# Performance work log

Measured on AMD Instinct MI355X. Metric: run time of the kernel, lower is better.

## Reference

```python
import jax, jax.numpy as jnp
import numpy as np


def apply_rope(x):
    # x: [b, h, n, d], d even
    b, h, n, d = x.shape
    half = d // 2
    freqs = jnp.arange(0, half, dtype=x.dtype) / half
    theta = 1.0 / 10000 ** freqs                       # [half]
    positions = jnp.arange(n, dtype=x.dtype)
    angles = positions[:, None] * theta[None, :]       # [n, half]
    cos = jnp.cos(angles)[None, None, :, :]
    sin = jnp.sin(angles)[None, None, :, :]
    x1 = x[..., ::2]
    x2 = x[..., 1::2]
    r1 = x1 * cos - x2 * sin
    r2 = x1 * sin + x2 * cos
    # interleave r1, r2 back into even/odd lanes
    return jnp.stack([r1, r2], axis=-1).reshape(b, h, n, d)


def setup_inputs() -> dict:
    key = jax.random.key(0)
    ks = jax.random.split(key, 4)
    B, N, D = 2, 2048, 1024
    x = jax.random.normal(ks[0], (B, N, D), dtype=jnp.float32)
    w_qkv = jax.random.normal(ks[1], (D, 3 * D), dtype=jnp.float32) * (1.0 / np.sqrt(D))
    b_qkv = jnp.zeros((3 * D,), dtype=jnp.float32)
    w_out = jax.random.normal(ks[2], (D, D), dtype=jnp.float32) * (1.0 / np.sqrt(D))
    b_out = jnp.zeros((D,), dtype=jnp.float32)
    return {"x": x, "w_qkv": w_qkv, "b_qkv": b_qkv, "w_out": w_out, "b_out": b_out}


def reference(x, w_qkv, b_qkv, w_out, b_out):
    B, N, D = x.shape
    H = 16
    hd = D // H
    qkv = x @ w_qkv + b_qkv                            # [B, N, 3D]
    q, k, v = jnp.split(qkv, 3, axis=-1)
    # [B, N, D] -> [B, H, N, hd]
    to_heads = lambda t: t.reshape(B, N, H, hd).transpose(0, 2, 1, 3)
    q, k, v = to_heads(q), to_heads(k), to_heads(v)
    # ELU+1 feature map (applied BEFORE RoPE, as in source)
    q = jax.nn.elu(q) + 1
    k = jax.nn.elu(k) + 1
    rot_q = apply_rope(q)
    rot_k = apply_rope(k)
    attn_num = jnp.einsum('bhid,bhjd->bhij', rot_q, rot_k)   # [B,H,N,N]
    attn_denom = jnp.einsum('bhid,bhjd->bhij', q, k)         # [B,H,N,N]
    attn_weights = attn_num / attn_denom
    # dropout deterministic (train=False)
    out = jnp.einsum('bhij,bhjd->bhid', attn_weights, v)     # [B,H,N,hd]
    out = out.transpose(0, 2, 1, 3).reshape(B, N, D)
    return out @ w_out + b_out
```

## Files before the change

kernel.cpp:

```cpp
#include <hip/hip_runtime.h>
#include <hip/hip_bf16.h>

#define B_   2
#define N_   2048
#define D_   1024
#define H_   16
#define HD   64
#define HALF 32
#define M_   (B_*N_)
#define DQKV (3*D_)

typedef __bf16 bf16x8 __attribute__((ext_vector_type(8)));
typedef float  f32x4  __attribute__((ext_vector_type(4)));
typedef float  f32x16 __attribute__((ext_vector_type(16)));

__device__ __forceinline__ bf16x8 ldfrag(const char* tile, int row, int ch) {
    return *(const bf16x8*)(tile + row * 128 + (((ch) ^ (row & 7)) << 4));
}
__device__ __forceinline__ void stfrag16(char* tile, int row, int ch, uint4 v) {
    *(uint4*)(tile + row * 128 + (((ch) ^ (row & 7)) << 4)) = v;
}

__device__ __forceinline__ unsigned pack2(float a, float b) {
    union { __hip_bfloat16 h; unsigned short s; } x, y;
    x.h = __float2bfloat16(a); y.h = __float2bfloat16(b);
    return (unsigned)x.s | ((unsigned)y.s << 16);
}

__global__ __launch_bounds__(256) void k_tables(float* __restrict__ cos_t,
                                                float* __restrict__ sin_t) {
    int i = blockIdx.x * 256 + threadIdx.x;
    if (i >= N_ * HALF) return;
    int n = i / HALF, j = i % HALF;
    float theta = powf(10000.f, -(float)j / (float)HALF);
    float ang = (float)n * theta;
    cos_t[i] = cosf(ang);
    sin_t[i] = sinf(ang);
}

__global__ __launch_bounds__(256) void k_cvt_x(const float* __restrict__ x,
                                               __hip_bfloat16* __restrict__ xb) {
    int i = blockIdx.x * 256 + threadIdx.x;
    float4 v = ((const float4*)x)[i];
    union { ushort4 u; __hip_bfloat16 h[4]; } o;
    o.h[0] = __float2bfloat16(v.x); o.h[1] = __float2bfloat16(v.y);
    o.h[2] = __float2bfloat16(v.z); o.h[3] = __float2bfloat16(v.w);
    ((ushort4*)xb)[i] = o.u;
}

__global__ __launch_bounds__(256) void k_cvt_t(const float* __restrict__ w,
                                               __hip_bfloat16* __restrict__ wt, int ncols) {
    __shared__ float tile[32][33];
    int n0 = blockIdx.x * 32, k0 = blockIdx.y * 32;
    int tx = threadIdx.x & 31, ty = threadIdx.x >> 5;
#pragma unroll
    for (int i = 0; i < 32; i += 8)
        tile[ty + i][tx] = w[(size_t)(k0 + ty + i) * ncols + n0 + tx];
    __syncthreads();
#pragma unroll
    for (int i = 0; i < 32; i += 8)
        wt[(size_t)(n0 + ty + i) * 1024 + k0 + tx] = __float2bfloat16(tile[tx][ty + i]);
}

__global__ __launch_bounds__(256) void k_qkv(
        const __hip_bfloat16* __restrict__ xb, const __hip_bfloat16* __restrict__ wqT,
        const float* __restrict__ bias,
        const float* __restrict__ cos_t, const float* __restrict__ sin_t,
        __hip_bfloat16* __restrict__ qf, __hip_bfloat16* __restrict__ kf,
        __hip_bfloat16* __restrict__ rq, __hip_bfloat16* __restrict__ rk,
        __hip_bfloat16* __restrict__ vt) {
    __shared__ __align__(16) char sA[128 * 128];
    __shared__ __align__(16) char sB[128 * 128];

    const int t    = threadIdx.x;
    const int m0   = blockIdx.y * 128;
    const int n0w  = blockIdx.x * 128;
    const int lane = t & 63;
    const int lrow = lane & 15;
    const int lgrp = lane >> 4;
    const int wid  = t >> 6;
    const int wr   = wid >> 1;
    const int wc   = wid & 1;

    f32x4 acc[4][4] = {};

    for (int kt = 0; kt < D_ / 64; ++kt) {
        const int k0 = kt * 64;
        __syncthreads();
#pragma unroll
        for (int it = 0; it < 4; ++it) {
            int slot = it * 256 + t;
            int r = slot >> 3, c = slot & 7;
            uint4 av = *(const uint4*)(xb  + (size_t)(m0  + r) * D_ + k0 + c * 8);
            uint4 bv = *(const uint4*)(wqT + (size_t)(n0w + r) * D_ + k0 + c * 8);
            stfrag16(sA, r, c, av);
            stfrag16(sB, r, c, bv);
        }
        __syncthreads();

        bf16x8 bfr[4][2];
#pragma unroll
        for (int fn = 0; fn < 4; ++fn) {
            bfr[fn][0] = ldfrag(sB, wc * 64 + fn * 16 + lrow, lgrp);
            bfr[fn][1] = ldfrag(sB, wc * 64 + fn * 16 + lrow, 4 + lgrp);
        }
#pragma unroll
        for (int fm = 0; fm < 4; ++fm) {
            bf16x8 a0 = ldfrag(sA, wr * 64 + fm * 16 + lrow, lgrp);
            bf16x8 a1 = ldfrag(sA, wr * 64 + fm * 16 + lrow, 4 + lgrp);
#pragma unroll
            for (int fn = 0; fn < 4; ++fn) {
                acc[fm][fn] = __builtin_amdgcn_mfma_f32_16x16x32_bf16(a0, bfr[fn][0], acc[fm][fn], 0, 0, 0);
                acc[fm][fn] = __builtin_amdgcn_mfma_f32_16x16x32_bf16(a1, bfr[fn][1], acc[fm][fn], 0, 0, 0);
            }
        }
    }

#pragma unroll
    for (int fn = 0; fn < 4; ++fn) {
        int c   = n0w + wc * 64 + fn * 16 + lrow;
        int sec = c >> 10;
        int cc  = c & 1023;
        int h   = cc >> 6, dd = cc & 63;
        float bia = bias[c];
#pragma unroll
        for (int fm = 0; fm < 4; ++fm) {
            int mb = m0 + wr * 64 + fm * 16 + lgrp * 4;
            int b  = mb >> 11;
            int n  = mb & (N_ - 1);
            if (sec == 2) {
                union { ushort4 u; __hip_bfloat16 hh[4]; } pk;
#pragma unroll
                for (int r = 0; r < 4; ++r)
                    pk.hh[r] = __float2bfloat16(acc[fm][fn][r] + bia);
                *(ushort4*)(vt + ((size_t)(b * H_ + h) * HD + dd) * N_ + n) = pk.u;
            } else {
#pragma unroll
                for (int r = 0; r < 4; ++r) {
                    float val = acc[fm][fn][r] + bia;
                    float e  = val > 0.f ? val + 1.f : __expf(val);
                    float ep = __shfl_xor(e, 1);
                    int pj = dd >> 1;
                    float cs = cos_t[(n + r) * HALF + pj];
                    float sn = sin_t[(n + r) * HALF + pj];
                    float rv = (dd & 1) ? (ep * sn + e * cs) : (e * cs - ep * sn);
                    size_t o = ((size_t)(b * H_ + h) * N_ + n + r) * HD + dd;
                    if (sec == 0) { qf[o] = __float2bfloat16(e); rq[o] = __float2bfloat16(rv); }
                    else          { kf[o] = __float2bfloat16(e); rk[o] = __float2bfloat16(rv); }
                }
            }
        }
    }
}

__global__ __launch_bounds__(256, 1) void k_attn(
        const __hip_bfloat16* __restrict__ qf, const __hip_bfloat16* __restrict__ kf,
        const __hip_bfloat16* __restrict__ rq, const __hip_bfloat16* __restrict__ rk,
        const __hip_bfloat16* __restrict__ vt, __hip_bfloat16* __restrict__ ctxb) {
    __shared__ __align__(16) char sbuf[2][3 * 8192];

    const int t    = threadIdx.x;
    const int lane = t & 63;
    const int l31  = lane & 31;
    const int h    = lane >> 5;
    const int w    = t >> 6;

    const int bid = blockIdx.x;
    const int swz = (bid & 7) * 32 + (bid >> 3);
    const int bh  = swz >> 3;
    const int q0  = (swz & 7) * 256;
    const size_t base = (size_t)bh * (N_ * HD);
    const int q0w = q0 + w * 64;

    bf16x8 bq[2][4], bqe[2][4];
#pragma unroll
    for (int qb = 0; qb < 2; ++qb)
#pragma unroll
        for (int kc = 0; kc < 4; ++kc) {
            int row = q0w + qb * 32 + l31;
            int col = kc * 16 + h * 8;
            bq [qb][kc] = *(const bf16x8*)(rq + base + (size_t)row * HD + col);
            bqe[qb][kc] = *(const bf16x8*)(qf + base + (size_t)row * HD + col);
        }

    uint4 st[6];
    {
#pragma unroll
        for (int it = 0; it < 6; ++it) {
            int slot = it * 256 + t, ci = slot & 511, row = ci >> 3, cs = ci & 7;
            int cg = cs ^ (row & 7);
            const char* g;
            if (it < 2)      g = (const char*)(rk + base + (size_t)row * HD) + cg * 16;
            else if (it < 4) g = (const char*)(kf + base + (size_t)row * HD) + cg * 16;
            else             g = (const char*)(vt + base + (size_t)row * N_) + cg * 16;
            st[it] = *(const uint4*)g;
        }
#pragma unroll
        for (int it = 0; it < 6; ++it) {
            int slot = it * 256 + t, ci = slot & 511, row = ci >> 3, cs = ci & 7;
            *(uint4*)(sbuf[0] + (it >> 1) * 8192 + row * 128 + cs * 16) = st[it];
        }
    }
    __syncthreads();

    f32x16 o[2][2] = {};

    for (int kt = 0; kt < 32; ++kt) {
        const int cur = kt & 1;
        const char* Rk = sbuf[cur];
        const char* Ke = sbuf[cur] + 8192;
        const char* Vt = sbuf[cur] + 16384;

        if (kt + 1 < 32) {
            const int k0n = (kt + 1) * 64;
#pragma unroll
            for (int it = 0; it < 6; ++it) {
                int slot = it * 256 + t, ci = slot & 511, row = ci >> 3, cs = ci & 7;
                int cg = cs ^ (row & 7);
                const char* g;
                if (it < 2)      g = (const char*)(rk + base + (size_t)(k0n + row) * HD) + cg * 16;
                else if (it < 4) g = (const char*)(kf + base + (size_t)(k0n + row) * HD) + cg * 16;
                else             g = (const char*)(vt + base + (size_t)row * N_ + k0n) + cg * 16;
                st[it] = *(const uint4*)g;
            }
        }

        bf16x8 wa[2][4];
#pragma unroll
        for (int qb = 0; qb < 2; ++qb) {
#pragma unroll
            for (int kb = 0; kb < 2; ++kb) {
                f32x16 num = {}, den = {};
#pragma unroll
                for (int kc = 0; kc < 4; ++kc) {
                    bf16x8 ark = ldfrag(Rk, kb * 32 + l31, kc * 2 + h);
                    num = __builtin_amdgcn_mfma_f32_32x32x16_bf16(ark, bq[qb][kc], num, 0, 0, 0);
                }
#pragma unroll
                for (int kc = 0; kc < 4; ++kc) {
                    bf16x8 ake = ldfrag(Ke, kb * 32 + l31, kc * 2 + h);
                    den = __builtin_amdgcn_mfma_f32_32x32x16_bf16(ake, bqe[qb][kc], den, 0, 0, 0);
                }
                unsigned u0 = pack2(num[0]  * __builtin_amdgcn_rcpf(den[0]),
                                    num[1]  * __builtin_amdgcn_rcpf(den[1]));
                unsigned u1 = pack2(num[2]  * __builtin_amdgcn_rcpf(den[2]),
                                    num[3]  * __builtin_amdgcn_rcpf(den[3]));
                unsigned u2 = pack2(num[4]  * __builtin_amdgcn_rcpf(den[4]),
                                    num[5]  * __builtin_amdgcn_rcpf(den[5]));
                unsigned u3 = pack2(num[6]  * __builtin_amdgcn_rcpf(den[6]),
                                    num[7]  * __builtin_amdgcn_rcpf(den[7]));
                unsigned u4 = pack2(num[8]  * __builtin_amdgcn_rcpf(den[8]),
                                    num[9]  * __builtin_amdgcn_rcpf(den[9]));
                unsigned u5 = pack2(num[10] * __builtin_amdgcn_rcpf(den[10]),
                                    num[11] * __builtin_amdgcn_rcpf(den[11]));
                unsigned u6 = pack2(num[12] * __builtin_amdgcn_rcpf(den[12]),
                                    num[13] * __builtin_amdgcn_rcpf(den[13]));
                unsigned u7 = pack2(num[14] * __builtin_amdgcn_rcpf(den[14]),
                                    num[15] * __builtin_amdgcn_rcpf(den[15]));
                asm volatile("v_permlane32_swap_b32 %0, %1" : "+v"(u0), "+v"(u2));
                asm volatile("v_permlane32_swap_b32 %0, %1" : "+v"(u1), "+v"(u3));
                asm volatile("v_permlane32_swap_b32 %0, %1" : "+v"(u4), "+v"(u6));
                asm volatile("v_permlane32_swap_b32 %0, %1" : "+v"(u5), "+v"(u7));
                union { unsigned uu[4]; bf16x8 v; } f0, f1;
                f0.uu[0] = u0; f0.uu[1] = u1; f0.uu[2] = u2; f0.uu[3] = u3;
                f1.uu[0] = u4; f1.uu[1] = u5; f1.uu[2] = u6; f1.uu[3] = u7;
                wa[qb][kb * 2 + 0] = f0.v;
                wa[qb][kb * 2 + 1] = f1.v;
            }
        }

#pragma unroll
        for (int qb = 0; qb < 2; ++qb)
#pragma unroll
            for (int db = 0; db < 2; ++db)
#pragma unroll
                for (int kc = 0; kc < 4; ++kc) {
                    bf16x8 bv = ldfrag(Vt, db * 32 + l31, kc * 2 + h);
                    o[qb][db] = __builtin_amdgcn_mfma_f32_32x32x16_bf16(wa[qb][kc], bv, o[qb][db], 0, 0, 0);
                }

        if (kt + 1 < 32) {
#pragma unroll
            for (int it = 0; it < 6; ++it) {
                int slot = it * 256 + t, ci = slot & 511, row = ci >> 3, cs = ci & 7;
                *(uint4*)(sbuf[cur ^ 1] + (it >> 1) * 8192 + row * 128 + cs * 16) = st[it];
            }
        }
        __syncthreads();
    }

#pragma unroll
    for (int qb = 0; qb < 2; ++qb)
#pragma unroll
        for (int db = 0; db < 2; ++db)
#pragma unroll
            for (int r = 0; r < 16; ++r) {
                int qq = q0w + qb * 32 + (r & 3) + 8 * (r >> 2) + 4 * h;
                int dv = db * 32 + l31;
                ctxb[base + (size_t)qq * HD + dv] = __float2bfloat16(o[qb][db][r]);
            }
}

__global__ __launch_bounds__(256) void k_proj(
        const __hip_bfloat16* __restrict__ ctxb, const __hip_bfloat16* __restrict__ woT,
        const float* __restrict__ bias, float* __restrict__ out) {
    __shared__ __align__(16) char sA[128 * 128];
    __shared__ __align__(16) char sB[128 * 128];

    const int t    = threadIdx.x;
    const int m0   = blockIdx.y * 128;
    const int n0w  = blockIdx.x * 128;
    const int lane = t & 63;
    const int lrow = lane & 15;
    const int lgrp = lane >> 4;
    const int wid  = t >> 6;
    const int wr   = wid >> 1;
    const int wc   = wid & 1;

    f32x4 acc[4][4] = {};

    for (int kt = 0; kt < D_ / 64; ++kt) {
        const int k0 = kt * 64;
        const int hh = k0 >> 6;
        __syncthreads();
#pragma unroll
        for (int it = 0; it < 4; ++it) {
            int slot = it * 256 + t;
            int r = slot >> 3, c = slot & 7;
            int m = m0 + r;
            int b = m >> 11, n = m & (N_ - 1);
            uint4 av = *(const uint4*)(ctxb + ((size_t)(b * H_ + hh) * N_ + n) * HD + c * 8);
            uint4 bv = *(const uint4*)(woT + (size_t)(n0w + r) * D_ + k0 + c * 8);
            stfrag16(sA, r, c, av);
            stfrag16(sB, r, c, bv);
        }
        __syncthreads();

        bf16x8 bfr[4][2];
#pragma unroll
        for (int fn = 0; fn < 4; ++fn) {
            bfr[fn][0] = ldfrag(sB, wc * 64 + fn * 16 + lrow, lgrp);
            bfr[fn][1] = ldfrag(sB, wc * 64 + fn * 16 + lrow, 4 + lgrp);
        }
#pragma unroll
        for (int fm = 0; fm < 4; ++fm) {
            bf16x8 a0 = ldfrag(sA, wr * 64 + fm * 16 + lrow, lgrp);
            bf16x8 a1 = ldfrag(sA, wr * 64 + fm * 16 + lrow, 4 + lgrp);
#pragma unroll
            for (int fn = 0; fn < 4; ++fn) {
                acc[fm][fn] = __builtin_amdgcn_mfma_f32_16x16x32_bf16(a0, bfr[fn][0], acc[fm][fn], 0, 0, 0);
                acc[fm][fn] = __builtin_amdgcn_mfma_f32_16x16x32_bf16(a1, bfr[fn][1], acc[fm][fn], 0, 0, 0);
            }
        }
    }

#pragma unroll
    for (int fn = 0; fn < 4; ++fn) {
        int c = n0w + wc * 64 + fn * 16 + lrow;
        float bia = bias[c];
#pragma unroll
        for (int fm = 0; fm < 4; ++fm) {
            int m = m0 + wr * 64 + fm * 16 + lgrp * 4;
#pragma unroll
            for (int r = 0; r < 4; ++r)
                out[(size_t)(m + r) * D_ + c] = acc[fm][fn][r] + bia;
        }
    }
}

extern "C" void kernel_launch(void* const* d_in, const int* in_sizes, int n_in,
                              void* d_out, int out_size, void* d_ws, size_t ws_size,
                              hipStream_t stream) {
    const float* x     = (const float*)d_in[0];
    const float* w_qkv = (const float*)d_in[1];
    const float* b_qkv = (const float*)d_in[2];
    const float* w_out = (const float*)d_in[3];
    const float* b_out = (const float*)d_in[4];
    float* out = (float*)d_out;

    char* ws = (char*)d_ws;
    const size_t TAB  = (size_t)N_ * HALF * sizeof(float);
    const size_t HARR = (size_t)B_ * H_ * N_ * HD * 2;
    float* cos_t = (float*)ws;
    float* sin_t = (float*)(ws + TAB);
    char* p = ws + 2 * TAB;
    __hip_bfloat16* qf  = (__hip_bfloat16*)(p);            p += HARR;
    __hip_bfloat16* kf  = (__hip_bfloat16*)(p);            p += HARR;
    __hip_bfloat16* rq  = (__hip_bfloat16*)(p);            p += HARR;
    __hip_bfloat16* rk  = (__hip_bfloat16*)(p);            p += HARR;
    __hip_bfloat16* vt  = (__hip_bfloat16*)(p);            p += HARR;
    __hip_bfloat16* xb  = (__hip_bfloat16*)(p);            p += HARR;
    __hip_bfloat16* ctxb = xb;
    __hip_bfloat16* wqT = (__hip_bfloat16*)(p);            p += (size_t)DQKV * D_ * 2;
    __hip_bfloat16* woT = (__hip_bfloat16*)(p);            p += (size_t)D_ * D_ * 2;

    hipLaunchKernelGGL(k_tables, dim3((N_ * HALF + 255) / 256), dim3(256), 0, stream,
                       cos_t, sin_t);
    hipLaunchKernelGGL(k_cvt_x, dim3(M_ * D_ / 4 / 256), dim3(256), 0, stream, x, xb);
    hipLaunchKernelGGL(k_cvt_t, dim3(DQKV / 32, D_ / 32), dim3(256), 0, stream,
                       w_qkv, wqT, DQKV);
    hipLaunchKernelGGL(k_cvt_t, dim3(D_ / 32, D_ / 32), dim3(256), 0, stream,
                       w_out, woT, D_);
    hipLaunchKernelGGL(k_qkv, dim3(DQKV / 128, M_ / 128), dim3(256), 0, stream,
                       xb, wqT, b_qkv, cos_t, sin_t, qf, kf, rq, rk, vt);
    hipLaunchKernelGGL(k_attn, dim3(256), dim3(256), 0, stream,
                       qf, kf, rq, rk, vt, ctxb);
    hipLaunchKernelGGL(k_proj, dim3(D_ / 128, M_ / 128), dim3(256), 0, stream,
                       ctxb, woT, b_out, out);
}
```

Baseline: 188.5 us.

## Split attention key range across warps, load K/V fragments directly from global

The attention kernel now launches twice as many blocks, each covering 128 queries. Two warps per query tile split the key range between them (split-K), and their partial outputs are combined through shared memory at the end. The double-buffered shared-memory staging of K/V tiles and its per-iteration barriers are removed. MFMA fragments are now read straight from global memory (via cache), and launch bounds allow two blocks per CU, aiming for more parallelism and occupancy. In exchange, K/V reuse across warps now relies on L1/L2 instead of LDS, and loads are less coalesced.

```diff
diff --git a/kernel.cpp b/kernel.cpp
--- a/kernel.cpp
+++ b/kernel.cpp
@@ -153,24 +153,26 @@
     }
 }
 
-__global__ __launch_bounds__(256, 1) void k_attn(
+__global__ __launch_bounds__(256, 2) void k_attn(
         const __hip_bfloat16* __restrict__ qf, const __hip_bfloat16* __restrict__ kf,
         const __hip_bfloat16* __restrict__ rq, const __hip_bfloat16* __restrict__ rk,
         const __hip_bfloat16* __restrict__ vt, __hip_bfloat16* __restrict__ ctxb) {
-    __shared__ __align__(16) char sbuf[2][3 * 8192];
+    __shared__ float sred[2][4096];
 
     const int t    = threadIdx.x;
     const int lane = t & 63;
     const int l31  = lane & 31;
     const int h    = lane >> 5;
     const int w    = t >> 6;
+    const int qw   = w & 1;
+    const int ks   = w >> 1;
 
     const int bid = blockIdx.x;
-    const int swz = (bid & 7) * 32 + (bid >> 3);
-    const int bh  = swz >> 3;
-    const int q0  = (swz & 7) * 256;
+    const int swz = (bid & 7) * 64 + (bid >> 3);
+    const int bh  = swz >> 4;
+    const int q0  = (swz & 15) * 128;
     const size_t base = (size_t)bh * (N_ * HD);
-    const int q0w = q0 + w * 64;
+    const int q0w = q0 + qw * 64;
 
     bf16x8 bq[2][4], bqe[2][4];
 #pragma unroll
@@ -183,64 +185,31 @@
             bqe[qb][kc] = *(const bf16x8*)(qf + base + (size_t)row * HD + col);
         }
 
-    uint4 st[6];
-    {
-#pragma unroll
-        for (int it = 0; it < 6; ++it) {
-            int slot = it * 256 + t, ci = slot & 511, row = ci >> 3, cs = ci & 7;
-            int cg = cs ^ (row & 7);
-            const char* g;
-            if (it < 2)      g = (const char*)(rk + base + (size_t)row * HD) + cg * 16;
-            else if (it < 4) g = (const char*)(kf + base + (size_t)row * HD) + cg * 16;
-            else             g = (const char*)(vt + base + (size_t)row * N_) + cg * 16;
-            st[it] = *(const uint4*)g;
-        }
-#pragma unroll
-        for (int it = 0; it < 6; ++it) {
-            int slot = it * 256 + t, ci = slot & 511, row = ci >> 3, cs = ci & 7;
-            *(uint4*)(sbuf[0] + (it >> 1) * 8192 + row * 128 + cs * 16) = st[it];
-        }
-    }
-    __syncthreads();
-
     f32x16 o[2][2] = {};
 
-    for (int kt = 0; kt < 32; ++kt) {
-        const int cur = kt & 1;
-        const char* Rk = sbuf[cur];
-        const char* Ke = sbuf[cur] + 8192;
-        const char* Vt = sbuf[cur] + 16384;
-
-        if (kt + 1 < 32) {
-            const int k0n = (kt + 1) * 64;
-#pragma unroll
-            for (int it = 0; it < 6; ++it) {
-                int slot = it * 256 + t, ci = slot & 511, row = ci >> 3, cs = ci & 7;
-                int cg = cs ^ (row & 7);
-                const char* g;
-                if (it < 2)      g = (const char*)(rk + base + (size_t)(k0n + row) * HD) + cg * 16;
-                else if (it < 4) g = (const char*)(kf + base + (size_t)(k0n + row) * HD) + cg * 16;
-                else             g = (const char*)(vt + base + (size_t)row * N_ + k0n) + cg * 16;
-                st[it] = *(const uint4*)g;
-            }
-        }
+    for (int r = 0; r < 16; ++r) {
+        const int k0 = (2 * r + ks) * 64;
+        const __hip_bfloat16* pk = rk + base + (size_t)k0 * HD + h * 8;
+        const __hip_bfloat16* pe = kf + base + (size_t)k0 * HD + h * 8;
 
         bf16x8 wa[2][4];
 #pragma unroll
-        for (int qb = 0; qb < 2; ++qb) {
-#pragma unroll
-            for (int kb = 0; kb < 2; ++kb) {
+        for (int kb = 0; kb < 2; ++kb) {
+            bf16x8 ark[4], ake[4];
+#pragma unroll
+            for (int kc = 0; kc < 4; ++kc) {
+                ark[kc] = *(const bf16x8*)(pk + (size_t)(kb * 32 + l31) * HD + kc * 16);
+                ake[kc] = *(const bf16x8*)(pe + (size_t)(kb * 32 + l31) * HD + kc * 16);
+            }
+#pragma unroll
+            for (int qb = 0; qb < 2; ++qb) {
                 f32x16 num = {}, den = {};
 #pragma unroll
-                for (int kc = 0; kc < 4; ++kc) {
-                    bf16x8 ark = ldfrag(Rk, kb * 32 + l31, kc * 2 + h);
-                    num = __builtin_amdgcn_mfma_f32_32x32x16_bf16(ark, bq[qb][kc], num, 0, 0, 0);
-                }
-#pragma unroll
-                for (int kc = 0; kc < 4; ++kc) {
-                    bf16x8 ake = ldfrag(Ke, kb * 32 + l31, kc * 2 + h);
-                    den = __builtin_amdgcn_mfma_f32_32x32x16_bf16(ake, bqe[qb][kc], den, 0, 0, 0);
-                }
+                for (int kc = 0; kc < 4; ++kc)
+                    num = __builtin_amdgcn_mfma_f32_32x32x16_bf16(ark[kc], bq[qb][kc], num, 0, 0, 0);
+#pragma unroll
+                for (int kc = 0; kc < 4; ++kc)
+                    den = __builtin_amdgcn_mfma_f32_32x32x16_bf16(ake[kc], bqe[qb][kc], den, 0, 0, 0);
                 unsigned u0 = pack2(num[0]  * __builtin_amdgcn_rcpf(den[0]),
                                     num[1]  * __builtin_amdgcn_rcpf(den[1]));
                 unsigned u1 = pack2(num[2]  * __builtin_amdgcn_rcpf(den[2]),
@@ -270,35 +239,42 @@
         }
 
 #pragma unroll
+        for (int db = 0; db < 2; ++db) {
+            bf16x8 bv[4];
+#pragma unroll
+            for (int kc = 0; kc < 4; ++kc)
+                bv[kc] = *(const bf16x8*)(vt + base + (size_t)(db * 32 + l31) * N_
+                                          + k0 + (kc * 2 + h) * 8);
+#pragma unroll
+            for (int qb = 0; qb < 2; ++qb)
+#pragma unroll
+                for (int kc = 0; kc < 4; ++kc)
+                    o[qb][db] = __builtin_amdgcn_mfma_f32_32x32x16_bf16(wa[qb][kc], bv[kc], o[qb][db], 0, 0, 0);
+        }
+    }
+
+    if (ks == 1) {
+#pragma unroll
         for (int qb = 0; qb < 2; ++qb)
 #pragma unroll
             for (int db = 0; db < 2; ++db)
 #pragma unroll
-                for (int kc = 0; kc < 4; ++kc) {
-                    bf16x8 bv = ldfrag(Vt, db * 32 + l31, kc * 2 + h);
-                    o[qb][db] = __builtin_amdgcn_mfma_f32_32x32x16_bf16(wa[qb][kc], bv, o[qb][db], 0, 0, 0);
+                for (int i = 0; i < 16; ++i)
+                    sred[qw][(qb * 2 + db) * 1024 + i * 64 + lane] = o[qb][db][i];
+    }
+    __syncthreads();
+    if (ks == 0) {
+#pragma unroll
+        for (int qb = 0; qb < 2; ++qb)
+#pragma unroll
+            for (int db = 0; db < 2; ++db)
+#pragma unroll
+                for (int i = 0; i < 16; ++i) {
+                    float v = o[qb][db][i] + sred[qw][(qb * 2 + db) * 1024 + i * 64 + lane];
+                    int qq = q0w + qb * 32 + (i & 3) + 8 * (i >> 2) + 4 * h;
+                    ctxb[base + (size_t)qq * HD + db * 32 + l31] = __float2bfloat16(v);
                 }
-
-        if (kt + 1 < 32) {
-#pragma unroll
-            for (int it = 0; it < 6; ++it) {
-                int slot = it * 256 + t, ci = slot & 511, row = ci >> 3, cs = ci & 7;
-                *(uint4*)(sbuf[cur ^ 1] + (it >> 1) * 8192 + row * 128 + cs * 16) = st[it];
-            }
-        }
-        __syncthreads();
-    }
-
-#pragma unroll
-    for (int qb = 0; qb < 2; ++qb)
-#pragma unroll
-        for (int db = 0; db < 2; ++db)
-#pragma unroll
-            for (int r = 0; r < 16; ++r) {
-                int qq = q0w + qb * 32 + (r & 3) + 8 * (r >> 2) + 4 * h;
-                int dv = db * 32 + l31;
-                ctxb[base + (size_t)qq * HD + dv] = __float2bfloat16(o[qb][db][r]);
-            }
+    }
 }
 
 __global__ __launch_bounds__(256) void k_proj(
@@ -403,7 +379,7 @@
                        w_out, woT, D_);
     hipLaunchKernelGGL(k_qkv, dim3(DQKV / 128, M_ / 128), dim3(256), 0, stream,
                        xb, wqT, b_qkv, cos_t, sin_t, qf, kf, rq, rk, vt);
-    hipLaunchKernelGGL(k_attn, dim3(256), dim3(256), 0, stream,
+    hipLaunchKernelGGL(k_attn, dim3(512), dim3(256), 0, stream,
                        qf, kf, rq, rk, vt, ctxb);
     hipLaunchKernelGGL(k_proj, dim3(D_ / 128, M_ / 128), dim3(256), 0, stream,
                        ctxb, woT, b_out, out);
```

After: 193.6 us. 1.03x slower.

## Halve attention query tile to 128 rows and double grid to 512 blocks

Applied to the files above, without the earlier changes.

Each attention block now handles 128 query rows (32 per wave) instead of 256, so the grid grows from 256 to 512 blocks and launch bounds allow two blocks per CU. With 256 blocks on a 256-CU part, each CU held a single block and had little latency hiding; the smaller tile lowers register pressure and adds occupancy. LDS fragments are also loaded in batches before the MFMA chains. The trade-off is that every K/V tile is loaded from global memory twice as often across the grid, and each wave gets less MFMA reuse per LDS read.

```diff
diff --git a/kernel.cpp b/kernel.cpp
--- a/kernel.cpp
+++ b/kernel.cpp
@@ -153,7 +153,7 @@
     }
 }
 
-__global__ __launch_bounds__(256, 1) void k_attn(
+__global__ __launch_bounds__(256, 2) void k_attn(
         const __hip_bfloat16* __restrict__ qf, const __hip_bfloat16* __restrict__ kf,
         const __hip_bfloat16* __restrict__ rq, const __hip_bfloat16* __restrict__ rk,
         const __hip_bfloat16* __restrict__ vt, __hip_bfloat16* __restrict__ ctxb) {
@@ -166,22 +166,20 @@
     const int w    = t >> 6;
 
     const int bid = blockIdx.x;
-    const int swz = (bid & 7) * 32 + (bid >> 3);
-    const int bh  = swz >> 3;
-    const int q0  = (swz & 7) * 256;
+    const int swz = (bid & 7) * 64 + (bid >> 3);
+    const int bh  = swz >> 4;
+    const int q0  = (swz & 15) * 128;
     const size_t base = (size_t)bh * (N_ * HD);
-    const int q0w = q0 + w * 64;
-
-    bf16x8 bq[2][4], bqe[2][4];
-#pragma unroll
-    for (int qb = 0; qb < 2; ++qb)
-#pragma unroll
-        for (int kc = 0; kc < 4; ++kc) {
-            int row = q0w + qb * 32 + l31;
-            int col = kc * 16 + h * 8;
-            bq [qb][kc] = *(const bf16x8*)(rq + base + (size_t)row * HD + col);
-            bqe[qb][kc] = *(const bf16x8*)(qf + base + (size_t)row * HD + col);
-        }
+    const int q0w = q0 + w * 32;
+
+    bf16x8 bq[4], bqe[4];
+#pragma unroll
+    for (int kc = 0; kc < 4; ++kc) {
+        int row = q0w + l31;
+        int col = kc * 16 + h * 8;
+        bq [kc] = *(const bf16x8*)(rq + base + (size_t)row * HD + col);
+        bqe[kc] = *(const bf16x8*)(qf + base + (size_t)row * HD + col);
+    }
 
     uint4 st[6];
     {
@@ -203,7 +201,7 @@
     }
     __syncthreads();
 
-    f32x16 o[2][2] = {};
+    f32x16 o[2] = {};
 
     for (int kt = 0; kt < 32; ++kt) {
         const int cur = kt & 1;
@@ -225,59 +223,59 @@
             }
         }
 
-        bf16x8 wa[2][4];
-#pragma unroll
-        for (int qb = 0; qb < 2; ++qb) {
-#pragma unroll
-            for (int kb = 0; kb < 2; ++kb) {
-                f32x16 num = {}, den = {};
-#pragma unroll
-                for (int kc = 0; kc < 4; ++kc) {
-                    bf16x8 ark = ldfrag(Rk, kb * 32 + l31, kc * 2 + h);
-                    num = __builtin_amdgcn_mfma_f32_32x32x16_bf16(ark, bq[qb][kc], num, 0, 0, 0);
-                }
-#pragma unroll
-                for (int kc = 0; kc < 4; ++kc) {
-                    bf16x8 ake = ldfrag(Ke, kb * 32 + l31, kc * 2 + h);
-                    den = __builtin_amdgcn_mfma_f32_32x32x16_bf16(ake, bqe[qb][kc], den, 0, 0, 0);
-                }
-                unsigned u0 = pack2(num[0]  * __builtin_amdgcn_rcpf(den[0]),
-                                    num[1]  * __builtin_amdgcn_rcpf(den[1]));
-                unsigned u1 = pack2(num[2]  * __builtin_amdgcn_rcpf(den[2]),
-                                    num[3]  * __builtin_amdgcn_rcpf(den[3]));
-                unsigned u2 = pack2(num[4]  * __builtin_amdgcn_rcpf(den[4]),
-                                    num[5]  * __builtin_amdgcn_rcpf(den[5]));
-                unsigned u3 = pack2(num[6]  * __builtin_amdgcn_rcpf(den[6]),
-                                    num[7]  * __builtin_amdgcn_rcpf(den[7]));
-                unsigned u4 = pack2(num[8]  * __builtin_amdgcn_rcpf(den[8]),
-                                    num[9]  * __builtin_amdgcn_rcpf(den[9]));
-                unsigned u5 = pack2(num[10] * __builtin_amdgcn_rcpf(den[10]),
-                                    num[11] * __builtin_amdgcn_rcpf(den[11]));
-                unsigned u6 = pack2(num[12] * __builtin_amdgcn_rcpf(den[12]),
-                                    num[13] * __builtin_amdgcn_rcpf(den[13]));
-                unsigned u7 = pack2(num[14] * __builtin_amdgcn_rcpf(den[14]),
-                                    num[15] * __builtin_amdgcn_rcpf(den[15]));
-                asm volatile("v_permlane32_swap_b32 %0, %1" : "+v"(u0), "+v"(u2));
-                asm volatile("v_permlane32_swap_b32 %0, %1" : "+v"(u1), "+v"(u3));
-                asm volatile("v_permlane32_swap_b32 %0, %1" : "+v"(u4), "+v"(u6));
-                asm volatile("v_permlane32_swap_b32 %0, %1" : "+v"(u5), "+v"(u7));
-                union { unsigned uu[4]; bf16x8 v; } f0, f1;
-                f0.uu[0] = u0; f0.uu[1] = u1; f0.uu[2] = u2; f0.uu[3] = u3;
-                f1.uu[0] = u4; f1.uu[1] = u5; f1.uu[2] = u6; f1.uu[3] = u7;
-                wa[qb][kb * 2 + 0] = f0.v;
-                wa[qb][kb * 2 + 1] = f1.v;
-            }
-        }
-
-#pragma unroll
-        for (int qb = 0; qb < 2; ++qb)
-#pragma unroll
-            for (int db = 0; db < 2; ++db)
-#pragma unroll
-                for (int kc = 0; kc < 4; ++kc) {
-                    bf16x8 bv = ldfrag(Vt, db * 32 + l31, kc * 2 + h);
-                    o[qb][db] = __builtin_amdgcn_mfma_f32_32x32x16_bf16(wa[qb][kc], bv, o[qb][db], 0, 0, 0);
-                }
+        bf16x8 wa[4];
+#pragma unroll
+        for (int kb = 0; kb < 2; ++kb) {
+            bf16x8 ark[4], ake[4];
+#pragma unroll
+            for (int kc = 0; kc < 4; ++kc) {
+                ark[kc] = ldfrag(Rk, kb * 32 + l31, kc * 2 + h);
+                ake[kc] = ldfrag(Ke, kb * 32 + l31, kc * 2 + h);
+            }
+            f32x16 num = {}, den = {};
+#pragma unroll
+            for (int kc = 0; kc < 4; ++kc)
+                num = __builtin_amdgcn_mfma_f32_32x32x16_bf16(ark[kc], bq[kc], num, 0, 0, 0);
+#pragma unroll
+            for (int kc = 0; kc < 4; ++kc)
+                den = __builtin_amdgcn_mfma_f32_32x32x16_bf16(ake[kc], bqe[kc], den, 0, 0, 0);
+            unsigned u0 = pack2(num[0]  * __builtin_amdgcn_rcpf(den[0]),
+                                num[1]  * __builtin_amdgcn_rcpf(den[1]));
+            unsigned u1 = pack2(num[2]  * __builtin_amdgcn_rcpf(den[2]),
+                                num[3]  * __builtin_amdgcn_rcpf(den[3]));
+            unsigned u2 = pack2(num[4]  * __builtin_amdgcn_rcpf(den[4]),
+                                num[5]  * __builtin_amdgcn_rcpf(den[5]));
+            unsigned u3 = pack2(num[6]  * __builtin_amdgcn_rcpf(den[6]),
+                                num[7]  * __builtin_amdgcn_rcpf(den[7]));
+            unsigned u4 = pack2(num[8]  * __builtin_amdgcn_rcpf(den[8]),
+                                num[9]  * __builtin_amdgcn_rcpf(den[9]));
+            unsigned u5 = pack2(num[10] * __builtin_amdgcn_rcpf(den[10]),
+                                num[11] * __builtin_amdgcn_rcpf(den[11]));
+            unsigned u6 = pack2(num[12] * __builtin_amdgcn_rcpf(den[12]),
+                                num[13] * __builtin_amdgcn_rcpf(den[13]));
+            unsigned u7 = pack2(num[14] * __builtin_amdgcn_rcpf(den[14]),
+                                num[15] * __builtin_amdgcn_rcpf(den[15]));
+            asm volatile("v_permlane32_swap_b32 %0, %1" : "+v"(u0), "+v"(u2));
+            asm volatile("v_permlane32_swap_b32 %0, %1" : "+v"(u1), "+v"(u3));
+            asm volatile("v_permlane32_swap_b32 %0, %1" : "+v"(u4), "+v"(u6));
+            asm volatile("v_permlane32_swap_b32 %0, %1" : "+v"(u5), "+v"(u7));
+            union { unsigned uu[4]; bf16x8 v; } f0, f1;
+            f0.uu[0] = u0; f0.uu[1] = u1; f0.uu[2] = u2; f0.uu[3] = u3;
+            f1.uu[0] = u4; f1.uu[1] = u5; f1.uu[2] = u6; f1.uu[3] = u7;
+            wa[kb * 2 + 0] = f0.v;
+            wa[kb * 2 + 1] = f1.v;
+        }
+
+#pragma unroll
+        for (int db = 0; db < 2; ++db) {
+            bf16x8 bv[4];
+#pragma unroll
+            for (int kc = 0; kc < 4; ++kc)
+                bv[kc] = ldfrag(Vt, db * 32 + l31, kc * 2 + h);
+#pragma unroll
+            for (int kc = 0; kc < 4; ++kc)
+                o[db] = __builtin_amdgcn_mfma_f32_32x32x16_bf16(wa[kc], bv[kc], o[db], 0, 0, 0);
+        }
 
         if (kt + 1 < 32) {
 #pragma unroll
@@ -290,15 +288,12 @@
     }
 
 #pragma unroll
-    for (int qb = 0; qb < 2; ++qb)
-#pragma unroll
-        for (int db = 0; db < 2; ++db)
-#pragma unroll
-            for (int r = 0; r < 16; ++r) {
-                int qq = q0w + qb * 32 + (r & 3) + 8 * (r >> 2) + 4 * h;
-                int dv = db * 32 + l31;
-                ctxb[base + (size_t)qq * HD + dv] = __float2bfloat16(o[qb][db][r]);
-            }
+    for (int db = 0; db < 2; ++db)
+#pragma unroll
+        for (int i = 0; i < 16; ++i) {
+            int qq = q0w + (i & 3) + 8 * (i >> 2) + 4 * h;
+            ctxb[base + (size_t)qq * HD + db * 32 + l31] = __float2bfloat16(o[db][i]);
+        }
 }
 
 __global__ __launch_bounds__(256) void k_proj(
@@ -403,7 +398,7 @@
                        w_out, woT, D_);
     hipLaunchKernelGGL(k_qkv, dim3(DQKV / 128, M_ / 128), dim3(256), 0, stream,
                        xb, wqT, b_qkv, cos_t, sin_t, qf, kf, rq, rk, vt);
-    hipLaunchKernelGGL(k_attn, dim3(256), dim3(256), 0, stream,
+    hipLaunchKernelGGL(k_attn, dim3(512), dim3(256), 0, stream,
                        qf, kf, rq, rk, vt, ctxb);
     hipLaunchKernelGGL(k_proj, dim3(D_ / 128, M_ / 128), dim3(256), 0, stream,
                        ctxb, woT, b_out, out);
```

Result: slower. 206.8 us (+9.7%).
